# Performance work log

Measured on AMD Instinct MI355X. Metric: run time of the kernel, lower is better.

## Reference

```python
import jax, jax.numpy as jnp
import numpy as np

WS = 8          # window size (Wh = Ww = 8)
N = WS * WS     # tokens per window = 64
DIM = 256
HEADS = 8
HEAD_DIM = DIM // HEADS
BW = 8192       # num_windows * batch


def _relative_position_index(ws: int) -> np.ndarray:
    ch, cw = np.meshgrid(np.arange(ws), np.arange(ws), indexing='ij')
    coords = np.stack([ch, cw]).reshape(2, -1)                 # (2, N)
    rel = coords[:, :, None] - coords[:, None, :]              # (2, N, N)
    rel = rel.transpose(1, 2, 0).astype(np.int32)              # (N, N, 2)
    rel[:, :, 0] += ws - 1
    rel[:, :, 1] += ws - 1
    rel[:, :, 0] *= 2 * ws - 1
    return rel.sum(-1)                                         # (N, N)


def setup_inputs() -> dict:
    key = jax.random.key(0)
    k1, k2, k3, k4, k5, k6 = jax.random.split(key, 6)
    table_size = (2 * WS - 1) * (2 * WS - 1)                   # 225
    return {
        'x': jax.random.normal(k1, (BW, N, DIM), dtype=jnp.float32),
        'w_qkv': jax.random.normal(k2, (3 * DIM, DIM), dtype=jnp.float32) * 0.02,
        'b_qkv': jax.random.normal(k3, (3 * DIM,), dtype=jnp.float32) * 0.02,
        'w_proj': jax.random.normal(k4, (DIM, DIM), dtype=jnp.float32) * 0.02,
        'b_proj': jax.random.normal(k5, (DIM,), dtype=jnp.float32) * 0.02,
        'rpb_table': jax.random.normal(k6, (table_size, HEADS), dtype=jnp.float32) * 0.02,
        'rpi': jnp.asarray(_relative_position_index(WS)),      # (N, N) int32
    }


def reference(x, w_qkv, b_qkv, w_proj, b_proj, rpb_table, rpi):
    b_, n, c = x.shape
    scale = HEAD_DIM ** (-0.5)
    qkv = x @ w_qkv.T + b_qkv                                  # (b_, n, 3c)
    qkv = qkv.reshape(b_, n, 3, HEADS, HEAD_DIM).transpose(2, 0, 3, 1, 4)
    q, k, v = qkv[0], qkv[1], qkv[2]                           # each (b_, H, n, d)
    attn = jnp.einsum('bhnd,bhmd->bhnm', q * scale, k)         # (b_, H, n, n)
    bias = rpb_table[rpi.reshape(-1)].reshape(n, n, HEADS)     # (n, n, H)
    attn = attn + bias.transpose(2, 0, 1)[None]                # + (1, H, n, n)
    attn = jax.nn.softmax(attn, axis=-1)
    out = jnp.einsum('bhnm,bhmd->bhnd', attn, v)               # (b_, H, n, d)
    out = out.transpose(0, 2, 1, 3).reshape(b_, n, c)
    return out @ w_proj.T + b_proj
```

## Files before the change

### kernel.cpp

```cpp
#include <hip/hip_runtime.h>
#include <hip/hip_bf16.h>

typedef __bf16 bf16x8 __attribute__((ext_vector_type(8)));
typedef float f32x4 __attribute__((ext_vector_type(4)));
typedef unsigned short u16;
typedef u16 u16x4 __attribute__((ext_vector_type(4)));

__device__ __forceinline__ u16 bfbits(float f) {
  return __builtin_bit_cast(u16, (__bf16)f);
}

__global__ void wattn_prep(const float* __restrict__ wq, const float* __restrict__ wp,
                           const float* __restrict__ rpb, const int* __restrict__ rpi,
                           u16* __restrict__ wqb, u16* __restrict__ wpb,
                           float* __restrict__ biasb) {
  int i = blockIdx.x * blockDim.x + threadIdx.x;
  if (i < 196608) wqb[i] = bfbits(wq[i]);
  if (i < 65536)  wpb[i] = bfbits(wp[i]);
  if (i < 32768) {
    int h = i >> 12, nm = i & 4095;
    biasb[i] = rpb[rpi[nm] * 8 + h];
  }
}

__global__ __launch_bounds__(512, 4)
void wattn_main(const float* __restrict__ x,
                const u16* __restrict__ wq, const float* __restrict__ bq,
                const u16* __restrict__ wp, const float* __restrict__ bp,
                const float* __restrict__ bias,
                float* __restrict__ out) {
  extern __shared__ u16 sm[];
  u16* Xb = sm;
  u16* Ao = sm + 16896;

  const int b    = blockIdx.x;
  const int tid  = threadIdx.x;
  const int w    = tid >> 6;
  const int lane = tid & 63;
  const int g    = lane >> 4;
  const int li   = lane & 15;
  const int hc   = 32 * w;

  {
    const float4* xg = (const float4*)(x + (size_t)b * 16384);
    #pragma unroll
    for (int i = 0; i < 8; ++i) {
      int idx = tid + i * 512;
      float4 v = xg[idx];
      int n = idx >> 6, c = (idx & 63) * 4;
      u16x4 h;
      h[0] = bfbits(v.x); h[1] = bfbits(v.y); h[2] = bfbits(v.z); h[3] = bfbits(v.w);
      *(u16x4*)(Xb + n * 264 + c) = h;
    }
  }
  __syncthreads();

  const int xoff = li * 264 + 8 * g;
  const float scale = 0.17677669529663687f;

  bf16x8 qf[4];
  {
    f32x4 aq[2][4];
    #pragma unroll
    for (int mt = 0; mt < 2; ++mt)
      #pragma unroll
      for (int nt = 0; nt < 4; ++nt) aq[mt][nt] = f32x4{0,0,0,0};
    #pragma unroll 2
    for (int ks = 0; ks < 8; ++ks) {
      bf16x8 xb[4];
      #pragma unroll
      for (int nt = 0; nt < 4; ++nt)
        xb[nt] = *(const bf16x8*)(Xb + xoff + nt * (16 * 264) + 32 * ks);
      #pragma unroll
      for (int mt = 0; mt < 2; ++mt) {
        bf16x8 wf = *(const bf16x8*)(wq + (hc + 16 * mt + li) * 256 + 32 * ks + 8 * g);
        #pragma unroll
        for (int nt = 0; nt < 4; ++nt)
          aq[mt][nt] = __builtin_amdgcn_mfma_f32_16x16x32_bf16(wf, xb[nt], aq[mt][nt], 0, 0, 0);
      }
    }
    #pragma unroll
    for (int j = 0; j < 8; ++j) {
      int d = (j < 4) ? (4 * g + j) : (16 + 4 * g + (j - 4));
      float bb = bq[hc + d];
      #pragma unroll
      for (int t = 0; t < 4; ++t)
        qf[t][j] = (__bf16)(((j < 4 ? aq[0][t][j] : aq[1][t][j - 4]) + bb) * scale);
    }
  }
  __builtin_amdgcn_sched_barrier(0);

  bf16x8 kf[4];
  {
    f32x4 ak[2][4];
    #pragma unroll
    for (int mt = 0; mt < 2; ++mt)
      #pragma unroll
      for (int nt = 0; nt < 4; ++nt) ak[mt][nt] = f32x4{0,0,0,0};
    #pragma unroll 2
    for (int ks = 0; ks < 8; ++ks) {
      bf16x8 xb[4];
      #pragma unroll
      for (int nt = 0; nt < 4; ++nt)
        xb[nt] = *(const bf16x8*)(Xb + xoff + nt * (16 * 264) + 32 * ks);
      #pragma unroll
      for (int mt = 0; mt < 2; ++mt) {
        bf16x8 wf = *(const bf16x8*)(wq + (256 + hc + 16 * mt + li) * 256 + 32 * ks + 8 * g);
        #pragma unroll
        for (int nt = 0; nt < 4; ++nt)
          ak[mt][nt] = __builtin_amdgcn_mfma_f32_16x16x32_bf16(wf, xb[nt], ak[mt][nt], 0, 0, 0);
      }
    }
    #pragma unroll
    for (int j = 0; j < 8; ++j) {
      int d = (j < 4) ? (4 * g + j) : (16 + 4 * g + (j - 4));
      float bb = bq[256 + hc + d];
      #pragma unroll
      for (int t = 0; t < 4; ++t)
        kf[t][j] = (__bf16)((j < 4 ? ak[0][t][j] : ak[1][t][j - 4]) + bb);
    }
  }
  __builtin_amdgcn_sched_barrier(0);

  bf16x8 vb[2][2];
  {
    f32x4 av[4][2];
    #pragma unroll
    for (int mt = 0; mt < 4; ++mt)
      #pragma unroll
      for (int nt = 0; nt < 2; ++nt) av[mt][nt] = f32x4{0,0,0,0};
    #pragma unroll 2
    for (int ks = 0; ks < 8; ++ks) {
      bf16x8 xb[4];
      #pragma unroll
      for (int mt = 0; mt < 4; ++mt)
        xb[mt] = *(const bf16x8*)(Xb + xoff + mt * (16 * 264) + 32 * ks);
      #pragma unroll
      for (int nt = 0; nt < 2; ++nt) {
        bf16x8 wf = *(const bf16x8*)(wq + (512 + hc + 16 * nt + li) * 256 + 32 * ks + 8 * g);
        #pragma unroll
        for (int mt = 0; mt < 4; ++mt)
          av[mt][nt] = __builtin_amdgcn_mfma_f32_16x16x32_bf16(xb[mt], wf, av[mt][nt], 0, 0, 0);
      }
    }
    #pragma unroll
    for (int nt = 0; nt < 2; ++nt) {
      float bb = bq[512 + hc + 16 * nt + li];
      #pragma unroll
      for (int kk = 0; kk < 2; ++kk)
        #pragma unroll
        for (int j = 0; j < 8; ++j)
          vb[kk][nt][j] = (__bf16)((j < 4 ? av[2 * kk][nt][j] : av[2 * kk + 1][nt][j - 4]) + bb);
    }
  }
  __builtin_amdgcn_sched_barrier(0);

  bf16x8 pa[4][2];
  {
    const float* bh = bias + w * 4096;
    #pragma unroll
    for (int ct = 0; ct < 4; ++ct) {
      f32x4 s4[4];
      #pragma unroll
      for (int rt = 0; rt < 4; ++rt)
        s4[rt] = __builtin_amdgcn_mfma_f32_16x16x32_bf16(kf[rt], qf[ct], f32x4{0,0,0,0}, 0, 0, 0);
      const float* bq_row = bh + (16 * ct + li) * 64 + 4 * g;
      float mx = -1e30f;
      #pragma unroll
      for (int rt = 0; rt < 4; ++rt) {
        f32x4 bv = *(const f32x4*)(bq_row + 16 * rt);
        #pragma unroll
        for (int e = 0; e < 4; ++e) {
          s4[rt][e] += bv[e];
          mx = fmaxf(mx, s4[rt][e]);
        }
      }
      mx = fmaxf(mx, __shfl_xor(mx, 16));
      mx = fmaxf(mx, __shfl_xor(mx, 32));
      float sum = 0.f;
      #pragma unroll
      for (int rt = 0; rt < 4; ++rt)
        #pragma unroll
        for (int e = 0; e < 4; ++e) {
          float p = __expf(s4[rt][e] - mx);
          s4[rt][e] = p;
          sum += p;
        }
      sum += __shfl_xor(sum, 16);
      sum += __shfl_xor(sum, 32);
      float rs = 1.0f / sum;
      #pragma unroll
      for (int kk = 0; kk < 2; ++kk)
        #pragma unroll
        for (int j = 0; j < 8; ++j)
          pa[ct][kk][j] = (__bf16)((j < 4 ? s4[2 * kk][j] : s4[2 * kk + 1][j - 4]) * rs);
    }
  }
  __builtin_amdgcn_sched_barrier(0);

  f32x4 o[4][2];
  #pragma unroll
  for (int mt = 0; mt < 4; ++mt)
    #pragma unroll
    for (int nt = 0; nt < 2; ++nt) o[mt][nt] = f32x4{0,0,0,0};
  #pragma unroll
  for (int kk = 0; kk < 2; ++kk)
    #pragma unroll
    for (int mt = 0; mt < 4; ++mt)
      #pragma unroll
      for (int nt = 0; nt < 2; ++nt)
        o[mt][nt] = __builtin_amdgcn_mfma_f32_16x16x32_bf16(pa[mt][kk], vb[kk][nt], o[mt][nt], 0, 0, 0);

  #pragma unroll
  for (int mt = 0; mt < 4; ++mt)
    #pragma unroll
    for (int nt = 0; nt < 2; ++nt)
      #pragma unroll
      for (int e = 0; e < 4; ++e)
        Ao[(16 * mt + 4 * g + e) * 264 + hc + 16 * nt + li] = bfbits(o[mt][nt][e]);
  __syncthreads();

  f32x4 c2[4][2];
  #pragma unroll
  for (int rt = 0; rt < 4; ++rt)
    #pragma unroll
    for (int ct = 0; ct < 2; ++ct) c2[rt][ct] = f32x4{0,0,0,0};
  #pragma unroll 2
  for (int ks = 0; ks < 8; ++ks) {
    bf16x8 af[4];
    #pragma unroll
    for (int rt = 0; rt < 4; ++rt)
      af[rt] = *(const bf16x8*)(Ao + xoff + rt * (16 * 264) + 32 * ks);
    bf16x8 wf[2];
    #pragma unroll
    for (int ct = 0; ct < 2; ++ct)
      wf[ct] = *(const bf16x8*)(wp + (32 * w + 16 * ct + li) * 256 + 32 * ks + 8 * g);
    #pragma unroll
    for (int rt = 0; rt < 4; ++rt)
      #pragma unroll
      for (int ct = 0; ct < 2; ++ct)
        c2[rt][ct] = __builtin_amdgcn_mfma_f32_16x16x32_bf16(af[rt], wf[ct], c2[rt][ct], 0, 0, 0);
  }
  {
    float* og = out + (size_t)b * 16384;
    #pragma unroll
    for (int ct = 0; ct < 2; ++ct) {
      int col = 32 * w + 16 * ct + li;
      float bpv = bp[col];
      #pragma unroll
      for (int rt = 0; rt < 4; ++rt)
        #pragma unroll
        for (int e = 0; e < 4; ++e)
          og[(16 * rt + 4 * g + e) * 256 + col] = c2[rt][ct][e] + bpv;
    }
  }
}

extern "C" void kernel_launch(void* const* d_in, const int* in_sizes, int n_in,
                              void* d_out, int out_size, void* d_ws, size_t ws_size,
                              hipStream_t stream) {
  const float* x   = (const float*)d_in[0];
  const float* wqv = (const float*)d_in[1];
  const float* bq  = (const float*)d_in[2];
  const float* wpr = (const float*)d_in[3];
  const float* bp  = (const float*)d_in[4];
  const float* rpb = (const float*)d_in[5];
  const int*   rpi = (const int*)d_in[6];
  float* out = (float*)d_out;

  u16*   wqb   = (u16*)d_ws;
  u16*   wpb   = wqb + 196608;
  float* biasb = (float*)(wpb + 65536);

  wattn_prep<<<384, 512, 0, stream>>>(wqv, wpr, rpb, rpi, wqb, wpb, biasb);

  const size_t smem = (16896 + 16896) * sizeof(u16);
  hipFuncSetAttribute(reinterpret_cast<const void*>(wattn_main),
                      hipFuncAttributeMaxDynamicSharedMemorySize, (int)smem);
  wattn_main<<<8192, 512, smem, stream>>>(x, wqb, bq, wpb, bp, biasb, out);
}
```

Measured before the change: 760.2 us.

## Swizzle LDS layout, fuse Q/K projection loops, fold biases into MFMA accumulators

```diff
diff --git a/kernel.cpp b/kernel.cpp
--- a/kernel.cpp
+++ b/kernel.cpp
@@ -29,9 +29,9 @@
                 const u16* __restrict__ wp, const float* __restrict__ bp,
                 const float* __restrict__ bias,
                 float* __restrict__ out) {
-  extern __shared__ u16 sm[];
-  u16* Xb = sm;
-  u16* Ao = sm + 16896;
+  extern __shared__ char smc[];
+  char* Xb = smc;
+  char* Ao = smc + 33792;
 
   const int b    = blockIdx.x;
   const int tid  = threadIdx.x;
@@ -47,134 +47,72 @@
     for (int i = 0; i < 8; ++i) {
       int idx = tid + i * 512;
       float4 v = xg[idx];
-      int n = idx >> 6, c = (idx & 63) * 4;
+      int n = idx >> 6, cb = (idx & 63) << 3;
       u16x4 h;
       h[0] = bfbits(v.x); h[1] = bfbits(v.y); h[2] = bfbits(v.z); h[3] = bfbits(v.w);
-      *(u16x4*)(Xb + n * 264 + c) = h;
+      *(u16x4*)(Xb + n * 528 + (cb ^ ((n & 7) << 4))) = h;
     }
   }
   __syncthreads();
 
-  const int xoff = li * 264 + 8 * g;
+  const int swz = (li & 7) << 4;
+  const char* Xrow = Xb + li * 528;
   const float scale = 0.17677669529663687f;
 
-  bf16x8 qf[4];
-  {
-    f32x4 aq[2][4];
-    #pragma unroll
-    for (int mt = 0; mt < 2; ++mt)
-      #pragma unroll
-      for (int nt = 0; nt < 4; ++nt) aq[mt][nt] = f32x4{0,0,0,0};
+  bf16x8 qf[4], kf[4];
+  {
+    f32x4 aq[2][4], ak[2][4];
+    #pragma unroll
+    for (int mt = 0; mt < 2; ++mt) {
+      f32x4 bqv = *(const f32x4*)(bq + hc + 16 * mt + 4 * g);
+      f32x4 bkv = *(const f32x4*)(bq + 256 + hc + 16 * mt + 4 * g);
+      #pragma unroll
+      for (int nt = 0; nt < 4; ++nt) { aq[mt][nt] = bqv; ak[mt][nt] = bkv; }
+    }
     #pragma unroll 2
     for (int ks = 0; ks < 8; ++ks) {
       bf16x8 xb[4];
       #pragma unroll
       for (int nt = 0; nt < 4; ++nt)
-        xb[nt] = *(const bf16x8*)(Xb + xoff + nt * (16 * 264) + 32 * ks);
+        xb[nt] = *(const bf16x8*)(Xrow + nt * (16 * 528) + ((64 * ks + 16 * g) ^ swz));
       #pragma unroll
       for (int mt = 0; mt < 2; ++mt) {
-        bf16x8 wf = *(const bf16x8*)(wq + (hc + 16 * mt + li) * 256 + 32 * ks + 8 * g);
+        bf16x8 wfq = *(const bf16x8*)(wq + (hc + 16 * mt + li) * 256 + 32 * ks + 8 * g);
         #pragma unroll
         for (int nt = 0; nt < 4; ++nt)
-          aq[mt][nt] = __builtin_amdgcn_mfma_f32_16x16x32_bf16(wf, xb[nt], aq[mt][nt], 0, 0, 0);
-      }
-    }
-    #pragma unroll
-    for (int j = 0; j < 8; ++j) {
-      int d = (j < 4) ? (4 * g + j) : (16 + 4 * g + (j - 4));
-      float bb = bq[hc + d];
-      #pragma unroll
-      for (int t = 0; t < 4; ++t)
-        qf[t][j] = (__bf16)(((j < 4 ? aq[0][t][j] : aq[1][t][j - 4]) + bb) * scale);
-    }
+          aq[mt][nt] = __builtin_amdgcn_mfma_f32_16x16x32_bf16(wfq, xb[nt], aq[mt][nt], 0, 0, 0);
+        bf16x8 wfk = *(const bf16x8*)(wq + (256 + hc + 16 * mt + li) * 256 + 32 * ks + 8 * g);
+        #pragma unroll
+        for (int nt = 0; nt < 4; ++nt)
+          ak[mt][nt] = __builtin_amdgcn_mfma_f32_16x16x32_bf16(wfk, xb[nt], ak[mt][nt], 0, 0, 0);
+      }
+    }
+    #pragma unroll
+    for (int j = 0; j < 8; ++j)
+      #pragma unroll
+      for (int t = 0; t < 4; ++t) {
+        qf[t][j] = (__bf16)((j < 4 ? aq[0][t][j] : aq[1][t][j - 4]) * scale);
+        kf[t][j] = (__bf16)((j < 4 ? ak[0][t][j] : ak[1][t][j - 4]));
+      }
   }
   __builtin_amdgcn_sched_barrier(0);
 
-  bf16x8 kf[4];
-  {
-    f32x4 ak[2][4];
-    #pragma unroll
-    for (int mt = 0; mt < 2; ++mt)
-      #pragma unroll
-      for (int nt = 0; nt < 4; ++nt) ak[mt][nt] = f32x4{0,0,0,0};
-    #pragma unroll 2
-    for (int ks = 0; ks < 8; ++ks) {
-      bf16x8 xb[4];
-      #pragma unroll
-      for (int nt = 0; nt < 4; ++nt)
-        xb[nt] = *(const bf16x8*)(Xb + xoff + nt * (16 * 264) + 32 * ks);
-      #pragma unroll
-      for (int mt = 0; mt < 2; ++mt) {
-        bf16x8 wf = *(const bf16x8*)(wq + (256 + hc + 16 * mt + li) * 256 + 32 * ks + 8 * g);
-        #pragma unroll
-        for (int nt = 0; nt < 4; ++nt)
-          ak[mt][nt] = __builtin_amdgcn_mfma_f32_16x16x32_bf16(wf, xb[nt], ak[mt][nt], 0, 0, 0);
-      }
-    }
-    #pragma unroll
-    for (int j = 0; j < 8; ++j) {
-      int d = (j < 4) ? (4 * g + j) : (16 + 4 * g + (j - 4));
-      float bb = bq[256 + hc + d];
-      #pragma unroll
-      for (int t = 0; t < 4; ++t)
-        kf[t][j] = (__bf16)((j < 4 ? ak[0][t][j] : ak[1][t][j - 4]) + bb);
-    }
-  }
-  __builtin_amdgcn_sched_barrier(0);
-
-  bf16x8 vb[2][2];
-  {
-    f32x4 av[4][2];
-    #pragma unroll
-    for (int mt = 0; mt < 4; ++mt)
-      #pragma unroll
-      for (int nt = 0; nt < 2; ++nt) av[mt][nt] = f32x4{0,0,0,0};
-    #pragma unroll 2
-    for (int ks = 0; ks < 8; ++ks) {
-      bf16x8 xb[4];
-      #pragma unroll
-      for (int mt = 0; mt < 4; ++mt)
-        xb[mt] = *(const bf16x8*)(Xb + xoff + mt * (16 * 264) + 32 * ks);
-      #pragma unroll
-      for (int nt = 0; nt < 2; ++nt) {
-        bf16x8 wf = *(const bf16x8*)(wq + (512 + hc + 16 * nt + li) * 256 + 32 * ks + 8 * g);
-        #pragma unroll
-        for (int mt = 0; mt < 4; ++mt)
-          av[mt][nt] = __builtin_amdgcn_mfma_f32_16x16x32_bf16(xb[mt], wf, av[mt][nt], 0, 0, 0);
-      }
-    }
-    #pragma unroll
-    for (int nt = 0; nt < 2; ++nt) {
-      float bb = bq[512 + hc + 16 * nt + li];
-      #pragma unroll
-      for (int kk = 0; kk < 2; ++kk)
-        #pragma unroll
-        for (int j = 0; j < 8; ++j)
-          vb[kk][nt][j] = (__bf16)((j < 4 ? av[2 * kk][nt][j] : av[2 * kk + 1][nt][j - 4]) + bb);
-    }
-  }
-  __builtin_amdgcn_sched_barrier(0);
-
   bf16x8 pa[4][2];
   {
     const float* bh = bias + w * 4096;
     #pragma unroll
     for (int ct = 0; ct < 4; ++ct) {
+      const float* br = bh + (16 * ct + li) * 64 + 4 * g;
       f32x4 s4[4];
       #pragma unroll
       for (int rt = 0; rt < 4; ++rt)
-        s4[rt] = __builtin_amdgcn_mfma_f32_16x16x32_bf16(kf[rt], qf[ct], f32x4{0,0,0,0}, 0, 0, 0);
-      const float* bq_row = bh + (16 * ct + li) * 64 + 4 * g;
+        s4[rt] = __builtin_amdgcn_mfma_f32_16x16x32_bf16(kf[rt], qf[ct],
+                                                         *(const f32x4*)(br + 16 * rt), 0, 0, 0);
       float mx = -1e30f;
       #pragma unroll
-      for (int rt = 0; rt < 4; ++rt) {
-        f32x4 bv = *(const f32x4*)(bq_row + 16 * rt);
-        #pragma unroll
-        for (int e = 0; e < 4; ++e) {
-          s4[rt][e] += bv[e];
-          mx = fmaxf(mx, s4[rt][e]);
-        }
-      }
+      for (int rt = 0; rt < 4; ++rt)
+        #pragma unroll
+        for (int e = 0; e < 4; ++e) mx = fmaxf(mx, s4[rt][e]);
       mx = fmaxf(mx, __shfl_xor(mx, 16));
       mx = fmaxf(mx, __shfl_xor(mx, 32));
       float sum = 0.f;
@@ -198,11 +136,44 @@
   }
   __builtin_amdgcn_sched_barrier(0);
 
+  bf16x8 vb[2][2];
+  {
+    f32x4 av[4][2];
+    #pragma unroll
+    for (int nt = 0; nt < 2; ++nt) {
+      float bb = bq[512 + hc + 16 * nt + li];
+      #pragma unroll
+      for (int mt = 0; mt < 4; ++mt) av[mt][nt] = f32x4{bb, bb, bb, bb};
+    }
+    #pragma unroll 2
+    for (int ks = 0; ks < 8; ++ks) {
+      bf16x8 xbv[4];
+      #pragma unroll
+      for (int mt = 0; mt < 4; ++mt)
+        xbv[mt] = *(const bf16x8*)(Xrow + mt * (16 * 528) + ((64 * ks + 16 * g) ^ swz));
+      #pragma unroll
+      for (int nt = 0; nt < 2; ++nt) {
+        bf16x8 wf = *(const bf16x8*)(wq + (512 + hc + 16 * nt + li) * 256 + 32 * ks + 8 * g);
+        #pragma unroll
+        for (int mt = 0; mt < 4; ++mt)
+          av[mt][nt] = __builtin_amdgcn_mfma_f32_16x16x32_bf16(xbv[mt], wf, av[mt][nt], 0, 0, 0);
+      }
+    }
+    #pragma unroll
+    for (int nt = 0; nt < 2; ++nt)
+      #pragma unroll
+      for (int kk = 0; kk < 2; ++kk)
+        #pragma unroll
+        for (int j = 0; j < 8; ++j)
+          vb[kk][nt][j] = (__bf16)((j < 4 ? av[2 * kk][nt][j] : av[2 * kk + 1][nt][j - 4]));
+  }
+  __builtin_amdgcn_sched_barrier(0);
+
   f32x4 o[4][2];
   #pragma unroll
   for (int mt = 0; mt < 4; ++mt)
     #pragma unroll
-    for (int nt = 0; nt < 2; ++nt) o[mt][nt] = f32x4{0,0,0,0};
+    for (int nt = 0; nt < 2; ++nt) o[mt][nt] = f32x4{0, 0, 0, 0};
   #pragma unroll
   for (int kk = 0; kk < 2; ++kk)
     #pragma unroll
@@ -216,42 +187,49 @@
     #pragma unroll
     for (int nt = 0; nt < 2; ++nt)
       #pragma unroll
-      for (int e = 0; e < 4; ++e)
-        Ao[(16 * mt + 4 * g + e) * 264 + hc + 16 * nt + li] = bfbits(o[mt][nt][e]);
+      for (int e = 0; e < 4; ++e) {
+        int row = 16 * mt + 4 * g + e;
+        int cb = (hc + 16 * nt + li) * 2;
+        *(u16*)(Ao + row * 528 + (cb ^ (((4 * g + e) & 7) << 4))) = bfbits(o[mt][nt][e]);
+      }
   __syncthreads();
 
   f32x4 c2[4][2];
   #pragma unroll
-  for (int rt = 0; rt < 4; ++rt)
-    #pragma unroll
-    for (int ct = 0; ct < 2; ++ct) c2[rt][ct] = f32x4{0,0,0,0};
-  #pragma unroll 2
-  for (int ks = 0; ks < 8; ++ks) {
-    bf16x8 af[4];
-    #pragma unroll
-    for (int rt = 0; rt < 4; ++rt)
-      af[rt] = *(const bf16x8*)(Ao + xoff + rt * (16 * 264) + 32 * ks);
-    bf16x8 wf[2];
-    #pragma unroll
-    for (int ct = 0; ct < 2; ++ct)
-      wf[ct] = *(const bf16x8*)(wp + (32 * w + 16 * ct + li) * 256 + 32 * ks + 8 * g);
-    #pragma unroll
-    for (int rt = 0; rt < 4; ++rt)
+  for (int ct = 0; ct < 2; ++ct) {
+    float bb = bp[32 * w + 16 * ct + li];
+    #pragma unroll
+    for (int rt = 0; rt < 4; ++rt) c2[rt][ct] = f32x4{bb, bb, bb, bb};
+  }
+  {
+    const char* Arow = Ao + li * 528;
+    #pragma unroll 2
+    for (int ks = 0; ks < 8; ++ks) {
+      bf16x8 af[4];
+      #pragma unroll
+      for (int rt = 0; rt < 4; ++rt)
+        af[rt] = *(const bf16x8*)(Arow + rt * (16 * 528) + ((64 * ks + 16 * g) ^ swz));
+      bf16x8 wf[2];
       #pragma unroll
       for (int ct = 0; ct < 2; ++ct)
-        c2[rt][ct] = __builtin_amdgcn_mfma_f32_16x16x32_bf16(af[rt], wf[ct], c2[rt][ct], 0, 0, 0);
+        wf[ct] = *(const bf16x8*)(wp + (32 * w + 16 * ct + li) * 256 + 32 * ks + 8 * g);
+      #pragma unroll
+      for (int rt = 0; rt < 4; ++rt)
+        #pragma unroll
+        for (int ct = 0; ct < 2; ++ct)
+          c2[rt][ct] = __builtin_amdgcn_mfma_f32_16x16x32_bf16(af[rt], wf[ct], c2[rt][ct], 0, 0, 0);
+    }
   }
   {
     float* og = out + (size_t)b * 16384;
     #pragma unroll
     for (int ct = 0; ct < 2; ++ct) {
       int col = 32 * w + 16 * ct + li;
-      float bpv = bp[col];
       #pragma unroll
       for (int rt = 0; rt < 4; ++rt)
         #pragma unroll
         for (int e = 0; e < 4; ++e)
-          og[(16 * rt + 4 * g + e) * 256 + col] = c2[rt][ct][e] + bpv;
+          og[(16 * rt + 4 * g + e) * 256 + col] = c2[rt][ct][e];
     }
   }
 }
@@ -274,7 +252,7 @@
 
   wattn_prep<<<384, 512, 0, stream>>>(wqv, wpr, rpb, rpi, wqb, wpb, biasb);
 
-  const size_t smem = (16896 + 16896) * sizeof(u16);
+  const size_t smem = 67584;
   hipFuncSetAttribute(reinterpret_cast<const void*>(wattn_main),
                       hipFuncAttributeMaxDynamicSharedMemorySize, (int)smem);
   wattn_main<<<8192, 512, smem, stream>>>(x, wqb, bq, wpb, bp, biasb, out);
```

Result: faster. 735.7 us (-3.2%).
